# Optimization experiments

Measured on AMD Instinct MI355X. Metric: run time of the kernel, lower is better.

Reference implementation:

```python
import jax, jax.numpy as jnp
import numpy as np

B, N, C, H = 16, 577, 384, 6
ONE_DIM = 24
RPD = 2 * ONE_DIM - 1  # 47
NUM_CLS = 1
HEAD_DIM = C // H
SCALE = HEAD_DIM ** -0.5


def _build_rel_pos_index():
    # Faithful to the torch loop: tmp[dy - y + off, dx - x + off] with
    # torch's negative-index wraparound -> modulo RPD.
    off = ONE_DIM // 2
    qy = np.repeat(np.arange(ONE_DIM), ONE_DIM)  # (Np,) y of each query patch
    qx = np.tile(np.arange(ONE_DIM), ONE_DIM)    # (Np,) x of each query patch
    ky, kx = qy, qx                              # key patches use same grid
    ry = (ky[None, :] - qy[:, None] + off) % RPD
    rx = (kx[None, :] - qx[:, None] + off) % RPD
    return jnp.asarray(ry * RPD + rx, dtype=jnp.int32)  # (Np, Np)


def setup_inputs() -> dict:
    key = jax.random.key(0)
    k = jax.random.split(key, 6)
    x = jax.random.normal(k[0], (B, N, C), dtype=jnp.float32)
    qkv_w = jax.random.normal(k[1], (3 * C, C), dtype=jnp.float32) * 0.02
    qkv_b = jnp.zeros((3 * C,), dtype=jnp.float32)
    proj_w = jax.random.normal(k[2], (C, C), dtype=jnp.float32) * 0.02
    proj_b = jnp.zeros((C,), dtype=jnp.float32)
    rel_pos = jax.random.normal(k[3], (H, RPD * RPD), dtype=jnp.float32) * 0.02
    mask = jax.random.randint(k[4], (B, N, N), 0, 2, dtype=jnp.int32)
    return {
        "x": x, "qkv_w": qkv_w, "qkv_b": qkv_b,
        "proj_w": proj_w, "proj_b": proj_b, "rel_pos": rel_pos,
        "rel_pos_index": _build_rel_pos_index(),
        "mask": mask, "patch_attn": 1,
    }


def reference(x, qkv_w, qkv_b, proj_w, proj_b, rel_pos, rel_pos_index, mask, patch_attn):
    # qkv projection: torch Linear -> x @ W^T + b
    qkv = x @ qkv_w.T + qkv_b                               # (B, N, 3C)
    qkv = qkv.reshape(B, N, 3, H, HEAD_DIM).transpose(2, 0, 3, 1, 4)
    q, k, v = qkv[0], qkv[1], qkv[2]                        # (B, H, N, hd)

    attn = jnp.einsum("bhqd,bhkd->bhqk", q, k) * SCALE      # (B, H, N, N)

    if patch_attn:
        # gather per-head relative-position bias for patch tokens
        bias = rel_pos[:, rel_pos_index]                    # (H, Np, Np)
        attn = attn.at[:, :, NUM_CLS:, NUM_CLS:].add(bias)

    neg = jnp.finfo(attn.dtype).min
    attn = jnp.where(mask[:, None, :, :] == 0, neg, attn)   # broadcast over heads

    attn = jax.nn.softmax(attn, axis=-1)
    out = jnp.einsum("bhqk,bhkd->bhqd", attn, v)            # (B, H, N, hd)
    out = out.transpose(0, 2, 1, 3).reshape(B, N, C)
    out = out @ proj_w.T + proj_b
    return out
```

## Files before the change

kernel.cpp:

```cpp
#include <hip/hip_runtime.h>
#include <float.h>
#include <math.h>

#define NB 16
#define NN 577
#define NC 384
#define NH 6
#define ND 64
#define RPD2 2209
#define MTOT 9232
#define MPAD 9344
#define SCALE_ 0.125f
#define NEGBIG -3.0e38f
#define BSTRIDE 580
#define NKPAD 640

typedef __attribute__((ext_vector_type(8))) short bf16x8;
typedef __attribute__((ext_vector_type(4))) float f32x4;
typedef unsigned short u16;

#define MFMA16(a, b, c) __builtin_amdgcn_mfma_f32_16x16x32_bf16(a, b, c, 0, 0, 0)

#define SQA 3932160ull
#define OFF_QH 0ull
#define OFF_QL SQA
#define OFF_KH (2ull * SQA)
#define OFF_KL (3ull * SQA)
#define OFF_VTH (4ull * SQA)
#define OFF_VTL (5ull * SQA)
#define OFF_XH (6ull * SQA)
#define OFF_XL (6ull * SQA + 3588096ull)
#define OFF_WQH (6ull * SQA + 2ull * 3588096ull)
#define OFF_WQL (OFF_WQH + 442368ull)
#define OFF_WPH (OFF_WQL + 442368ull)
#define OFF_WPL (OFF_WPH + 147456ull)
#define OFF_BT  (OFF_WPL + 147456ull)
#define OFF_PM  (OFF_BT + 2007960ull)

static __device__ __forceinline__ u16 f2bf(float f) {
  unsigned u = __float_as_uint(f);
  u += 0x7fff + ((u >> 16) & 1);
  return (u16)(u >> 16);
}
static __device__ __forceinline__ float bf2f(u16 h) {
  return __uint_as_float((unsigned)h << 16);
}
static __device__ __forceinline__ void split2(float v, u16& hi, u16& lo) {
  hi = f2bf(v);
  lo = f2bf(v - bf2f(hi));
}
static __device__ __forceinline__ void gload16(const void* g, void* l) {
  __builtin_amdgcn_global_load_lds(
      (const __attribute__((address_space(1))) void*)g,
      (__attribute__((address_space(3))) void*)l, 16, 0, 0);
}

__global__ __launch_bounds__(256) void prep_k(
    const float* __restrict__ x, const float* __restrict__ wq,
    const float* __restrict__ wp, const int* __restrict__ mask,
    const float* __restrict__ rel_pos, const int* __restrict__ rel_idx,
    const int* __restrict__ patch, u16* __restrict__ ws)
{
  const int bidx = blockIdx.x;
  const int tid = threadIdx.x;

  if (bidx < 4080) {
    const int q = bidx * 256 + tid;
    float4 v = {0.f, 0.f, 0.f, 0.f};
    u16 *dh, *dl;
    if (q < 897024) {
      if (q < 886272) v = ((const float4*)x)[q];
      dh = ws + OFF_XH + 4ull * q;
      dl = ws + OFF_XL + 4ull * q;
    } else if (q < 1007616) {
      int t = q - 897024;
      v = ((const float4*)wq)[t];
      dh = ws + OFF_WQH + 4ull * t;
      dl = ws + OFF_WQL + 4ull * t;
    } else {
      int t = q - 1007616;
      v = ((const float4*)wp)[t];
      dh = ws + OFF_WPH + 4ull * t;
      dl = ws + OFF_WPL + 4ull * t;
    }
    ushort4 hh, ll;
    split2(v.x, hh.x, ll.x);
    split2(v.y, hh.y, ll.y);
    split2(v.z, hh.z, ll.z);
    split2(v.w, hh.w, ll.w);
    *(ushort4*)dh = hh;
    *(ushort4*)dl = ll;
  } else if (bidx < 6388) {
    unsigned* pm = (unsigned*)(ws + OFF_PM);
    const int pbid = bidx - 4080;
    const int wid = (pbid * 256 + tid) >> 6;
    const int lane = tid & 63;
    if (wid >= MTOT) return;
    const int* mr = mask + (size_t)wid * NN;
#pragma unroll
    for (int c = 0; c < 10; ++c) {
      int k = c * 64 + lane;
      int v = (k < NN) ? mr[k] : 0;
      unsigned long long bal = __ballot(v != 0);
      if (lane == 0) pm[wid * 20 + 2 * c] = (unsigned)bal;
      if (lane == 1) pm[wid * 20 + 2 * c + 1] = (unsigned)(bal >> 32);
    }
  } else {
    const int f = bidx - 6388;
    const int q = f % NN, h = f / NN;
    const int pa = *patch;
    u16* row = ws + OFF_BT + ((size_t)h * NN + q) * BSTRIDE;
    for (int kk = tid; kk < BSTRIDE; kk += 256) {
      float v = 0.f;
      if (pa && q >= 1 && kk >= 1 && kk < NN)
        v = rel_pos[h * RPD2 + rel_idx[(q - 1) * 576 + (kk - 1)]];
      row[kk] = f2bf(v);
    }
  }
}

__global__ __launch_bounds__(256, 5) void qkv_mfma_k(
    const u16* __restrict__ Xh, const u16* __restrict__ Xl,
    const u16* __restrict__ Wh, const u16* __restrict__ Wl,
    const float* __restrict__ bias, u16* __restrict__ ws)
{
  __shared__ u16 LB[16384];

#define pASH(bf) (LB + (bf) * 4096)
#define pASL(bf) (LB + 8192 + (bf) * 4096)

  const int tid = threadIdx.x;
  const int w = tid >> 6, l = tid & 63, lq = l & 15, lg = l >> 4;
  const int wm = (w >> 1) * 64, wn = (w & 1) * 32;

  const int o = blockIdx.x;
  const int xcd = o & 7, rank = o >> 3;
  const int wg = (xcd < 2) ? (xcd * 165 + rank)
                           : (330 + (xcd - 2) * 164 + rank);
  const int mb = (wg / 18) * 128;
  const int rbi = wg % 18;
  const int rb = rbi * 64;
  const int r0 = rb + wn;
  const int soff = (l >> 2) * 384 + (l & 3) * 8;

#define STAGE_A(k0_, bf_)                                                    \
  {                                                                          \
    _Pragma("unroll")                                                        \
    for (int j = 0; j < 2; ++j) {                                            \
      const int tr = 32 * w + 16 * j;                                        \
      const size_t ga = (size_t)(mb + tr) * 384 + (k0_) + soff;              \
      gload16(&Xh[ga], pASH(bf_) + tr * 32);                                 \
      gload16(&Xl[ga], pASL(bf_) + tr * 32);                                 \
    }                                                                        \
  }

  const size_t brow = (size_t)(r0 + lq) * 384 + 8 * lg;
#define BLOAD(k0_, BH_, BL_)                                                 \
  {                                                                          \
    _Pragma("unroll")                                                        \
    for (int nt = 0; nt < 2; ++nt) {                                         \
      BH_[nt] = *(const bf16x8*)&Wh[brow + (size_t)(16 * nt) * 384 + (k0_)]; \
      BL_[nt] = *(const bf16x8*)&Wl[brow + (size_t)(16 * nt) * 384 + (k0_)]; \
    }                                                                        \
  }

#define COMPUTE(bf_)                                                         \
  {                                                                          \
    _Pragma("unroll")                                                        \
    for (int mt = 0; mt < 4; ++mt) {                                         \
      bf16x8 ah = *(const bf16x8*)(pASH(bf_) + (wm + 16 * mt + lq) * 32 + 8 * lg); \
      bf16x8 al = *(const bf16x8*)(pASL(bf_) + (wm + 16 * mt + lq) * 32 + 8 * lg); \
      _Pragma("unroll")                                                      \
      for (int nt = 0; nt < 2; ++nt) {                                       \
        acc[mt][nt] = MFMA16(ah, bhf[nt], acc[mt][nt]);                      \
        acc[mt][nt] = MFMA16(ah, blf[nt], acc[mt][nt]);                      \
        acc[mt][nt] = MFMA16(al, bhf[nt], acc[mt][nt]);                      \
      }                                                                      \
    }                                                                        \
  }

  bf16x8 bhf[2], blf[2], nbh[2], nbl[2];
  BLOAD(0, bhf, blf);
  STAGE_A(0, 0);
  STAGE_A(32, 1);

  f32x4 acc[4][2];
#pragma unroll
  for (int nt = 0; nt < 2; ++nt) {
    float bv = bias[r0 + 16 * nt + lq];
#pragma unroll
    for (int mt = 0; mt < 4; ++mt) acc[mt][nt] = (f32x4){bv, bv, bv, bv};
  }

  for (int k = 0; k < 11; ++k) {
    asm volatile("s_waitcnt vmcnt(4)" ::: "memory");
    __builtin_amdgcn_sched_barrier(0);
    __builtin_amdgcn_s_barrier();
    __builtin_amdgcn_sched_barrier(0);
    const int bfb = k & 1;
    COMPUTE(bfb);
    __builtin_amdgcn_sched_barrier(0);
    __builtin_amdgcn_s_barrier();
    __builtin_amdgcn_sched_barrier(0);
    BLOAD(32 * (k + 1), nbh, nbl);
    if (k < 10) STAGE_A(32 * (k + 2), bfb);
#pragma unroll
    for (int nt = 0; nt < 2; ++nt) { bhf[nt] = nbh[nt]; blf[nt] = nbl[nt]; }
  }
  asm volatile("s_waitcnt vmcnt(0)" ::: "memory");
  __builtin_amdgcn_sched_barrier(0);
  __builtin_amdgcn_s_barrier();
  __builtin_amdgcn_sched_barrier(0);
  COMPUTE(1);

#undef COMPUTE
#undef BLOAD
#undef STAGE_A

  const int comp = rbi / 6;
  const int h = rbi % 6;

  if (comp != 2) {
#pragma unroll
    for (int mt = 0; mt < 4; ++mt)
#pragma unroll
      for (int r = 0; r < 4; ++r) {
        int m = mb + wm + 16 * mt + 4 * lg + r;
        if (m >= MTOT) continue;
        int bb = m / NN, nn = m - bb * NN;
        int bh = bb * NH + h;
#pragma unroll
        for (int nt = 0; nt < 2; ++nt) {
          int d = wn + 16 * nt + lq;
          float v = acc[mt][nt][r];
          u16 hi, lo;
          if (comp == 0) {
            v *= SCALE_;
            split2(v, hi, lo);
            size_t a = ((size_t)bh * NKPAD + nn) * 64 + d;
            ws[OFF_QH + a] = hi;
            ws[OFF_QL + a] = lo;
          } else {
            split2(v, hi, lo);
            size_t a = ((size_t)bh * NKPAD + nn) * 64 + d;
            ws[OFF_KH + a] = hi;
            ws[OFF_KL + a] = lo;
          }
        }
      }
  } else {
    __syncthreads();
    u16* scr = LB + w * 2304;
    const int mlane = mb + wm + l;
    const bool mv = mlane < MTOT;
    int bb = 0, nn = 0;
    if (mv) { bb = mlane / NN; nn = mlane - bb * NN; }
    const size_t vbase = (((size_t)(bb * NH + h) * 64 + wn)) * NKPAD + nn;

    for (int part = 0; part < 2; ++part) {
      u16* dst = ws + (part ? OFF_VTL : OFF_VTH);
#pragma unroll
      for (int nt = 0; nt < 2; ++nt)
#pragma unroll
        for (int mt = 0; mt < 4; ++mt) {
          ushort4 pk;
          u16 hi, lo;
          split2(acc[mt][nt][0], hi, lo); pk.x = part ? lo : hi;
          split2(acc[mt][nt][1], hi, lo); pk.y = part ? lo : hi;
          split2(acc[mt][nt][2], hi, lo); pk.z = part ? lo : hi;
          split2(acc[mt][nt][3], hi, lo); pk.w = part ? lo : hi;
          *(ushort4*)&scr[(16 * nt + lq) * 72 + 16 * mt + 4 * lg] = pk;
        }
      if (mv) {
        for (int i = 0; i < 32; ++i)
          dst[vbase + (size_t)i * NKPAD] = scr[i * 72 + l];
      }
    }
  }
#undef pASH
#undef pASL
}

__global__ __launch_bounds__(256, 2) void attn_k(
    const u16* __restrict__ Qh, const u16* __restrict__ Ql,
    const u16* __restrict__ Kh, const u16* __restrict__ Kl,
    const u16* __restrict__ Vth, const u16* __restrict__ Vtl,
    const u16* __restrict__ btbl, const unsigned* __restrict__ pm,
    u16* __restrict__ Oh, u16* __restrict__ Ol)
{
  __shared__ u16 Kth[2][4096], Ktl[2][4096];
  __shared__ u16 Vsh[2][4096], Vsl[2][4096];
  __shared__ u16 Ph[4][2048];

  const int tid = threadIdx.x;
  const int w = tid >> 6, l = tid & 63, lq = l & 15, lg = l >> 4;
  const int q0 = blockIdx.x * 128;
  const int h = blockIdx.y, b = blockIdx.z;
  const int bh = b * NH + h;
  const int qr0 = q0 + 32 * w + lq;
  const int qr1 = qr0 + 16;
  const int swz = (lq & 7) << 3;
  const int ln8 = l >> 3, lc8 = l & 7;
  const int koff = ln8 * 64 + ((lc8 ^ ln8) << 3);
  const int voff = ln8 * NKPAD + ((lc8 ^ ln8) << 3);

#define STAGE(ch, bf)                                                        \
  {                                                                          \
    const int kb_ = (ch) * 64;                                               \
    const size_t kgb = ((size_t)bh * NKPAD + kb_ + 16 * w) * 64 + koff;      \
    const size_t vgb = ((size_t)bh * 64 + 16 * w) * NKPAD + kb_ + voff;      \
    gload16(&Kh[kgb],              &Kth[bf][(16 * w) * 64]);                 \
    gload16(&Kh[kgb + 512],        &Kth[bf][(16 * w + 8) * 64]);             \
    gload16(&Kl[kgb],              &Ktl[bf][(16 * w) * 64]);                 \
    gload16(&Kl[kgb + 512],        &Ktl[bf][(16 * w + 8) * 64]);             \
    gload16(&Vth[vgb],             &Vsh[bf][(16 * w) * 64]);                 \
    gload16(&Vth[vgb + 8 * NKPAD], &Vsh[bf][(16 * w + 8) * 64]);             \
    gload16(&Vtl[vgb],             &Vsl[bf][(16 * w) * 64]);                 \
    gload16(&Vtl[vgb + 8 * NKPAD], &Vsl[bf][(16 * w + 8) * 64]);             \
  }

  STAGE(0, 0);

  const size_t qb0 = ((size_t)bh * NKPAD + qr0) * 64 + 8 * lg;
  const size_t qb1 = ((size_t)bh * NKPAD + qr1) * 64 + 8 * lg;
  bf16x8 q0h[2], q0l[2], q1h[2], q1l[2];
  q0h[0] = *(const bf16x8*)&Qh[qb0];
  q0h[1] = *(const bf16x8*)&Qh[qb0 + 32];
  q0l[0] = *(const bf16x8*)&Ql[qb0];
  q0l[1] = *(const bf16x8*)&Ql[qb0 + 32];
  q1h[0] = *(const bf16x8*)&Qh[qb1];
  q1h[1] = *(const bf16x8*)&Qh[qb1 + 32];
  q1l[0] = *(const bf16x8*)&Ql[qb1];
  q1l[1] = *(const bf16x8*)&Ql[qb1 + 32];

  const int gq0 = (qr0 < NN) ? qr0 : NN - 1;
  const int gq1 = (qr1 < NN) ? qr1 : NN - 1;
  const bool qv0 = qr0 < NN, qv1 = qr1 < NN;
  const unsigned* pmrow0 = pm + ((size_t)b * NN + gq0) * 20;
  const unsigned* pmrow1 = pm + ((size_t)b * NN + gq1) * 20;
  const size_t brow0 = ((size_t)h * NN + gq0) * BSTRIDE;
  const size_t brow1 = ((size_t)h * NN + gq1) * BSTRIDE;

  uint2 cM0, cM1, nM0, nM1;
  uint2 cB0[4], cB1[4], nB0[4], nB1[4];
  cM0 = *(const uint2*)&pmrow0[0];
  cM1 = *(const uint2*)&pmrow1[0];
#pragma unroll
  for (int t = 0; t < 4; ++t) {
    int kkb = 16 * t + 4 * lg;
    cB0[t] = (qv0 && kkb <= 576) ? *(const uint2*)&btbl[brow0 + kkb]
                                 : make_uint2(0u, 0u);
    cB1[t] = (qv1 && kkb <= 576) ? *(const uint2*)&btbl[brow1 + kkb]
                                 : make_uint2(0u, 0u);
  }

  float m_reg0 = NEGBIG, l_reg0 = 0.f;
  float m_reg1 = NEGBIG, l_reg1 = 0.f;
  f32x4 accO0[4] = {}, accO1[4] = {};

  for (int ch = 0; ch < 10; ++ch) {
    const int bf = ch & 1;
    __syncthreads();
    if (ch < 9) {
      nM0 = *(const uint2*)&pmrow0[2 * (ch + 1)];
      nM1 = *(const uint2*)&pmrow1[2 * (ch + 1)];
      const int kb2 = (ch + 1) * 64;
#pragma unroll
      for (int t = 0; t < 4; ++t) {
        int kkb = kb2 + 16 * t + 4 * lg;
        nB0[t] = (qv0 && kkb <= 576) ? *(const uint2*)&btbl[brow0 + kkb]
                                     : make_uint2(0u, 0u);
        nB1[t] = (qv1 && kkb <= 576) ? *(const uint2*)&btbl[brow1 + kkb]
                                     : make_uint2(0u, 0u);
      }
      STAGE(ch + 1, bf ^ 1);
    }

    unsigned long long m64_0 = (unsigned long long)cM0.x |
                               ((unsigned long long)cM0.y << 32);
    unsigned long long m64_1 = (unsigned long long)cM1.x |
                               ((unsigned long long)cM1.y << 32);

    float sv0[4][4], sv1[4][4];
    __builtin_amdgcn_s_setprio(1);
#pragma unroll
    for (int t = 0; t < 4; ++t) {
      f32x4 a0, a1;
      a0[0] = bf2f((u16)(cB0[t].x & 0xffff));
      a0[1] = bf2f((u16)(cB0[t].x >> 16));
      a0[2] = bf2f((u16)(cB0[t].y & 0xffff));
      a0[3] = bf2f((u16)(cB0[t].y >> 16));
      a1[0] = bf2f((u16)(cB1[t].x & 0xffff));
      a1[1] = bf2f((u16)(cB1[t].x >> 16));
      a1[2] = bf2f((u16)(cB1[t].y & 0xffff));
      a1[3] = bf2f((u16)(cB1[t].y >> 16));
      const int ar = (16 * t + lq) * 64;
#pragma unroll
      for (int ks = 0; ks < 2; ++ks) {
        const int c = (8 * lg + 32 * ks) ^ swz;
        bf16x8 ah = *(const bf16x8*)&Kth[bf][ar + c];
        bf16x8 al = *(const bf16x8*)&Ktl[bf][ar + c];
        a0 = MFMA16(ah, q0h[ks], a0);
        a0 = MFMA16(ah, q0l[ks], a0);
        a0 = MFMA16(al, q0h[ks], a0);
        a1 = MFMA16(ah, q1h[ks], a1);
        a1 = MFMA16(ah, q1l[ks], a1);
        a1 = MFMA16(al, q1h[ks], a1);
      }
#pragma unroll
      for (int r = 0; r < 4; ++r) { sv0[t][r] = a0[r]; sv1[t][r] = a1[r]; }
    }
    __builtin_amdgcn_s_setprio(0);

    {
      float cmax = NEGBIG;
#pragma unroll
      for (int t = 0; t < 4; ++t)
#pragma unroll
        for (int r = 0; r < 4; ++r) {
          int kl = 16 * t + 4 * lg + r;
          float s = ((m64_0 >> kl) & 1ull) ? sv0[t][r] : NEGBIG;
          sv0[t][r] = s;
          cmax = fmaxf(cmax, s);
        }
      cmax = fmaxf(cmax, __shfl_xor(cmax, 16));
      cmax = fmaxf(cmax, __shfl_xor(cmax, 32));
      float m_new = fmaxf(m_reg0, cmax);
      float fx = __expf(m_reg0 - m_new);
      float csum = 0.f;
#pragma unroll
      for (int t = 0; t < 4; ++t) {
        float e0 = __expf(sv0[t][0] - m_new);
        float e1 = __expf(sv0[t][1] - m_new);
        float e2 = __expf(sv0[t][2] - m_new);
        float e3 = __expf(sv0[t][3] - m_new);
        csum += e0 + e1 + e2 + e3;
        ushort4 ph;
        ph.x = f2bf(e0); ph.y = f2bf(e1); ph.z = f2bf(e2); ph.w = f2bf(e3);
        *(ushort4*)&Ph[w][lq * 64 + ((16 * t + 4 * lg) ^ swz)] = ph;
      }
      csum += __shfl_xor(csum, 16);
      csum += __shfl_xor(csum, 32);
      l_reg0 = l_reg0 * fx + csum;
      m_reg0 = m_new;
      float fxr[4];
#pragma unroll
      for (int r = 0; r < 4; ++r) fxr[r] = __shfl(fx, 4 * lg + r);
#pragma unroll
      for (int t = 0; t < 4; ++t) {
        accO0[t][0] *= fxr[0]; accO0[t][1] *= fxr[1];
        accO0[t][2] *= fxr[2]; accO0[t][3] *= fxr[3];
      }
    }
    {
      float cmax = NEGBIG;
#pragma unroll
      for (int t = 0; t < 4; ++t)
#pragma unroll
        for (int r = 0; r < 4; ++r) {
          int kl = 16 * t + 4 * lg + r;
          float s = ((m64_1 >> kl) & 1ull) ? sv1[t][r] : NEGBIG;
          sv1[t][r] = s;
          cmax = fmaxf(cmax, s);
        }
      cmax = fmaxf(cmax, __shfl_xor(cmax, 16));
      cmax = fmaxf(cmax, __shfl_xor(cmax, 32));
      float m_new = fmaxf(m_reg1, cmax);
      float fx = __expf(m_reg1 - m_new);
      float csum = 0.f;
#pragma unroll
      for (int t = 0; t < 4; ++t) {
        float e0 = __expf(sv1[t][0] - m_new);
        float e1 = __expf(sv1[t][1] - m_new);
        float e2 = __expf(sv1[t][2] - m_new);
        float e3 = __expf(sv1[t][3] - m_new);
        csum += e0 + e1 + e2 + e3;
        ushort4 ph;
        ph.x = f2bf(e0); ph.y = f2bf(e1); ph.z = f2bf(e2); ph.w = f2bf(e3);
        *(ushort4*)&Ph[w][(16 + lq) * 64 + ((16 * t + 4 * lg) ^ swz)] = ph;
      }
      csum += __shfl_xor(csum, 16);
      csum += __shfl_xor(csum, 32);
      l_reg1 = l_reg1 * fx + csum;
      m_reg1 = m_new;
      float fxr[4];
#pragma unroll
      for (int r = 0; r < 4; ++r) fxr[r] = __shfl(fx, 4 * lg + r);
#pragma unroll
      for (int t = 0; t < 4; ++t) {
        accO1[t][0] *= fxr[0]; accO1[t][1] *= fxr[1];
        accO1[t][2] *= fxr[2]; accO1[t][3] *= fxr[3];
      }
    }

    bf16x8 pa0[2], pa1[2];
#pragma unroll
    for (int ks = 0; ks < 2; ++ks) {
      int c = (8 * lg + 32 * ks) ^ swz;
      pa0[ks] = *(const bf16x8*)&Ph[w][lq * 64 + c];
      pa1[ks] = *(const bf16x8*)&Ph[w][(16 + lq) * 64 + c];
    }

    __builtin_amdgcn_s_setprio(1);
#pragma unroll
    for (int t = 0; t < 4; ++t) {
      const int vr = (16 * t + lq) * 64;
#pragma unroll
      for (int ks = 0; ks < 2; ++ks) {
        const int c = (8 * lg + 32 * ks) ^ swz;
        bf16x8 vh = *(const bf16x8*)&Vsh[bf][vr + c];
        bf16x8 vl = *(const bf16x8*)&Vsl[bf][vr + c];
        accO0[t] = MFMA16(pa0[ks], vh, accO0[t]);
        accO0[t] = MFMA16(pa0[ks], vl, accO0[t]);
        accO1[t] = MFMA16(pa1[ks], vh, accO1[t]);
        accO1[t] = MFMA16(pa1[ks], vl, accO1[t]);
      }
    }
    __builtin_amdgcn_s_setprio(0);

    if (ch < 9) {
      cM0 = nM0; cM1 = nM1;
#pragma unroll
      for (int t = 0; t < 4; ++t) { cB0[t] = nB0[t]; cB1[t] = nB1[t]; }
    }
  }
#undef STAGE

  float il0 = 1.f / l_reg0;
  float il1 = 1.f / l_reg1;
  float ilr0[4], ilr1[4];
#pragma unroll
  for (int r = 0; r < 4; ++r) {
    ilr0[r] = __shfl(il0, 4 * lg + r);
    ilr1[r] = __shfl(il1, 4 * lg + r);
  }
#pragma unroll
  for (int t = 0; t < 4; ++t)
#pragma unroll
    for (int r = 0; r < 4; ++r) {
      int g0 = q0 + 32 * w + 4 * lg + r;
      if (g0 < NN) {
        float v = accO0[t][r] * ilr0[r];
        u16 hi, lo;
        split2(v, hi, lo);
        size_t a = ((size_t)b * NN + g0) * NC + h * 64 + 16 * t + lq;
        Oh[a] = hi;
        Ol[a] = lo;
      }
      int g1 = g0 + 16;
      if (g1 < NN) {
        float v = accO1[t][r] * ilr1[r];
        u16 hi, lo;
        split2(v, hi, lo);
        size_t a = ((size_t)b * NN + g1) * NC + h * 64 + 16 * t + lq;
        Oh[a] = hi;
        Ol[a] = lo;
      }
    }
}

__global__ __launch_bounds__(256, 4) void proj_mfma_k(
    const u16* __restrict__ Ah, const u16* __restrict__ Al,
    const u16* __restrict__ Wh, const u16* __restrict__ Wl,
    const float* __restrict__ bias, float* __restrict__ out)
{
  __shared__ u16 Ash[2][2048], Asl[2][2048];

  const int tid = threadIdx.x;
  const int w = tid >> 6, l = tid & 63, lq = l & 15, lg = l >> 4;
  const int wm = (w >> 1) * 32, wn = (w & 1) * 32;
  const int mb = blockIdx.x * 64;
  const int rb = blockIdx.y * 64;
  const int r0 = rb + wn;
  const int soff = (l >> 2) * 384 + (l & 3) * 8;

#define STAGE_A(k0_, bf_)                                                    \
  {                                                                          \
    const int tr = 16 * w;                                                   \
    const size_t ga = (size_t)(mb + tr) * 384 + (k0_) + soff;                \
    gload16(&Ah[ga], &Ash[bf_][tr * 32]);                                    \
    gload16(&Al[ga], &Asl[bf_][tr * 32]);                                    \
  }

  const size_t brow = (size_t)(r0 + lq) * 384 + 8 * lg;
#define BLOAD(k0_, BH_, BL_)                                                 \
  {                                                                          \
    _Pragma("unroll")                                                        \
    for (int nt = 0; nt < 2; ++nt) {                                         \
      BH_[nt] = *(const bf16x8*)&Wh[brow + (size_t)(16 * nt) * 384 + (k0_)]; \
      BL_[nt] = *(const bf16x8*)&Wl[brow + (size_t)(16 * nt) * 384 + (k0_)]; \
    }                                                                        \
  }

#define COMPUTE(bf_)                                                         \
  {                                                                          \
    _Pragma("unroll")                                                        \
    for (int mt = 0; mt < 2; ++mt) {                                         \
      bf16x8 ah = *(const bf16x8*)&Ash[bf_][(wm + 16 * mt + lq) * 32 + 8 * lg]; \
      bf16x8 al = *(const bf16x8*)&Asl[bf_][(wm + 16 * mt + lq) * 32 + 8 * lg]; \
      _Pragma("unroll")                                                      \
      for (int nt = 0; nt < 2; ++nt) {                                       \
        acc[mt][nt] = MFMA16(ah, bhf[nt], acc[mt][nt]);                      \
        acc[mt][nt] = MFMA16(ah, blf[nt], acc[mt][nt]);                      \
        acc[mt][nt] = MFMA16(al, bhf[nt], acc[mt][nt]);                      \
      }                                                                      \
    }                                                                        \
  }

  bf16x8 bhf[2], blf[2], nbh[2], nbl[2];
  BLOAD(0, bhf, blf);
  STAGE_A(0, 0);
  STAGE_A(32, 1);

  f32x4 acc[2][2];
#pragma unroll
  for (int nt = 0; nt < 2; ++nt) {
    float bv = bias[r0 + 16 * nt + lq];
#pragma unroll
    for (int mt = 0; mt < 2; ++mt) acc[mt][nt] = (f32x4){bv, bv, bv, bv};
  }

  for (int k = 0; k < 11; ++k) {
    asm volatile("s_waitcnt vmcnt(2)" ::: "memory");
    __builtin_amdgcn_sched_barrier(0);
    __builtin_amdgcn_s_barrier();
    __builtin_amdgcn_sched_barrier(0);
    const int bfb = k & 1;
    COMPUTE(bfb);
    __builtin_amdgcn_sched_barrier(0);
    __builtin_amdgcn_s_barrier();
    __builtin_amdgcn_sched_barrier(0);
    BLOAD(32 * (k + 1), nbh, nbl);
    if (k < 10) STAGE_A(32 * (k + 2), bfb);
#pragma unroll
    for (int nt = 0; nt < 2; ++nt) { bhf[nt] = nbh[nt]; blf[nt] = nbl[nt]; }
  }
  asm volatile("s_waitcnt vmcnt(0)" ::: "memory");
  __builtin_amdgcn_sched_barrier(0);
  __builtin_amdgcn_s_barrier();
  __builtin_amdgcn_sched_barrier(0);
  COMPUTE(1);

#undef COMPUTE
#undef BLOAD
#undef STAGE_A

#pragma unroll
  for (int mt = 0; mt < 2; ++mt)
#pragma unroll
    for (int r = 0; r < 4; ++r) {
      int m = mb + wm + 16 * mt + 4 * lg + r;
      if (m >= MTOT) continue;
#pragma unroll
      for (int nt = 0; nt < 2; ++nt)
        out[(size_t)m * NC + r0 + 16 * nt + lq] = acc[mt][nt][r];
    }
}

extern "C" void kernel_launch(void* const* d_in, const int* in_sizes, int n_in,
                              void* d_out, int out_size, void* d_ws, size_t ws_size,
                              hipStream_t stream) {
  const float* x       = (const float*)d_in[0];
  const float* qkv_w   = (const float*)d_in[1];
  const float* qkv_b   = (const float*)d_in[2];
  const float* proj_w  = (const float*)d_in[3];
  const float* proj_b  = (const float*)d_in[4];
  const float* rel_pos = (const float*)d_in[5];
  const int*   rel_idx = (const int*)d_in[6];
  const int*   mask    = (const int*)d_in[7];
  const int*   patch   = (const int*)d_in[8];
  float* out = (float*)d_out;
  u16* W16 = (u16*)d_ws;

  unsigned* pmp = (unsigned*)(W16 + OFF_PM);
  u16* btblp = W16 + OFF_BT;

  prep_k<<<9850, 256, 0, stream>>>(x, qkv_w, proj_w, mask, rel_pos, rel_idx,
                                   patch, W16);
  qkv_mfma_k<<<1314, 256, 0, stream>>>(
      W16 + OFF_XH, W16 + OFF_XL, W16 + OFF_WQH, W16 + OFF_WQL, qkv_b, W16);
  attn_k<<<dim3(5, NH, NB), 256, 0, stream>>>(
      W16 + OFF_QH, W16 + OFF_QL, W16 + OFF_KH, W16 + OFF_KL,
      W16 + OFF_VTH, W16 + OFF_VTL, btblp, pmp,
      W16 + OFF_XH, W16 + OFF_XL);
  proj_mfma_k<<<dim3(146, 6), 256, 0, stream>>>(
      W16 + OFF_XH, W16 + OFF_XL, W16 + OFF_WPH, W16 + OFF_WPL, proj_b, out);
}
```

Measured before the change: 151.5 us.

## Move mask/bias prep into QKV GEMM launch and restructure GEMM k-loop pipelining

The mask bit-packing and relative-position bias table construction move from the prep kernel into extra blocks of the QKV GEMM launch, so they run alongside the GEMM instead of before it. The prep kernel now only splits x and the weights into bf16 hi/lo. Both GEMM kernels change their k-loop to a fully unrolled 12-step double buffer with one barrier per step, issuing the next tile's loads before computing the current one. The loop now waits for all loads to finish (vmcnt(0)) at each step, which reduces overlap between memory loads and MFMA work.

```diff
diff --git a/kernel.cpp b/kernel.cpp
--- a/kernel.cpp
+++ b/kernel.cpp
@@ -57,83 +57,85 @@
 
 __global__ __launch_bounds__(256) void prep_k(
     const float* __restrict__ x, const float* __restrict__ wq,
-    const float* __restrict__ wp, const int* __restrict__ mask,
+    const float* __restrict__ wp, u16* __restrict__ ws)
+{
+  const int q = blockIdx.x * 256 + threadIdx.x;
+  float4 v = {0.f, 0.f, 0.f, 0.f};
+  u16 *dh, *dl;
+  if (q < 897024) {
+    if (q < 886272) v = ((const float4*)x)[q];
+    dh = ws + OFF_XH + 4ull * q;
+    dl = ws + OFF_XL + 4ull * q;
+  } else if (q < 1007616) {
+    int t = q - 897024;
+    v = ((const float4*)wq)[t];
+    dh = ws + OFF_WQH + 4ull * t;
+    dl = ws + OFF_WQL + 4ull * t;
+  } else {
+    int t = q - 1007616;
+    v = ((const float4*)wp)[t];
+    dh = ws + OFF_WPH + 4ull * t;
+    dl = ws + OFF_WPL + 4ull * t;
+  }
+  ushort4 hh, ll;
+  split2(v.x, hh.x, ll.x);
+  split2(v.y, hh.y, ll.y);
+  split2(v.z, hh.z, ll.z);
+  split2(v.w, hh.w, ll.w);
+  *(ushort4*)dh = hh;
+  *(ushort4*)dl = ll;
+}
+
+__global__ __launch_bounds__(256, 5) void qkv_mfma_k(
+    const u16* __restrict__ Xh, const u16* __restrict__ Xl,
+    const u16* __restrict__ Wh, const u16* __restrict__ Wl,
+    const float* __restrict__ bias, const int* __restrict__ mask,
     const float* __restrict__ rel_pos, const int* __restrict__ rel_idx,
     const int* __restrict__ patch, u16* __restrict__ ws)
 {
-  const int bidx = blockIdx.x;
+  __shared__ u16 LB[16384];
+
+  const int bid = blockIdx.x;
   const int tid = threadIdx.x;
 
-  if (bidx < 4080) {
-    const int q = bidx * 256 + tid;
-    float4 v = {0.f, 0.f, 0.f, 0.f};
-    u16 *dh, *dl;
-    if (q < 897024) {
-      if (q < 886272) v = ((const float4*)x)[q];
-      dh = ws + OFF_XH + 4ull * q;
-      dl = ws + OFF_XL + 4ull * q;
-    } else if (q < 1007616) {
-      int t = q - 897024;
-      v = ((const float4*)wq)[t];
-      dh = ws + OFF_WQH + 4ull * t;
-      dl = ws + OFF_WQL + 4ull * t;
+  if (bid >= 1314) {
+    if (bid < 3622) {
+      unsigned* pm = (unsigned*)(ws + OFF_PM);
+      const int pbid = bid - 1314;
+      const int wid = (pbid * 256 + tid) >> 6;
+      const int lane = tid & 63;
+      if (wid >= MTOT) return;
+      const int* mr = mask + (size_t)wid * NN;
+#pragma unroll
+      for (int c = 0; c < 10; ++c) {
+        int k = c * 64 + lane;
+        int v = (k < NN) ? mr[k] : 0;
+        unsigned long long bal = __ballot(v != 0);
+        if (lane == 0) pm[wid * 20 + 2 * c] = (unsigned)bal;
+        if (lane == 1) pm[wid * 20 + 2 * c + 1] = (unsigned)(bal >> 32);
+      }
     } else {
-      int t = q - 1007616;
-      v = ((const float4*)wp)[t];
-      dh = ws + OFF_WPH + 4ull * t;
-      dl = ws + OFF_WPL + 4ull * t;
-    }
-    ushort4 hh, ll;
-    split2(v.x, hh.x, ll.x);
-    split2(v.y, hh.y, ll.y);
-    split2(v.z, hh.z, ll.z);
-    split2(v.w, hh.w, ll.w);
-    *(ushort4*)dh = hh;
-    *(ushort4*)dl = ll;
-  } else if (bidx < 6388) {
-    unsigned* pm = (unsigned*)(ws + OFF_PM);
-    const int pbid = bidx - 4080;
-    const int wid = (pbid * 256 + tid) >> 6;
-    const int lane = tid & 63;
-    if (wid >= MTOT) return;
-    const int* mr = mask + (size_t)wid * NN;
-#pragma unroll
-    for (int c = 0; c < 10; ++c) {
-      int k = c * 64 + lane;
-      int v = (k < NN) ? mr[k] : 0;
-      unsigned long long bal = __ballot(v != 0);
-      if (lane == 0) pm[wid * 20 + 2 * c] = (unsigned)bal;
-      if (lane == 1) pm[wid * 20 + 2 * c + 1] = (unsigned)(bal >> 32);
-    }
-  } else {
-    const int f = bidx - 6388;
-    const int q = f % NN, h = f / NN;
-    const int pa = *patch;
-    u16* row = ws + OFF_BT + ((size_t)h * NN + q) * BSTRIDE;
-    for (int kk = tid; kk < BSTRIDE; kk += 256) {
-      float v = 0.f;
-      if (pa && q >= 1 && kk >= 1 && kk < NN)
-        v = rel_pos[h * RPD2 + rel_idx[(q - 1) * 576 + (kk - 1)]];
-      row[kk] = f2bf(v);
-    }
-  }
-}
-
-__global__ __launch_bounds__(256, 5) void qkv_mfma_k(
-    const u16* __restrict__ Xh, const u16* __restrict__ Xl,
-    const u16* __restrict__ Wh, const u16* __restrict__ Wl,
-    const float* __restrict__ bias, u16* __restrict__ ws)
-{
-  __shared__ u16 LB[16384];
+      const int f = bid - 3622;
+      const int q = f % NN, h = f / NN;
+      const int pa = *patch;
+      u16* row = ws + OFF_BT + ((size_t)h * NN + q) * BSTRIDE;
+      for (int kk = tid; kk < BSTRIDE; kk += 256) {
+        float v = 0.f;
+        if (pa && q >= 1 && kk >= 1 && kk < NN)
+          v = rel_pos[h * RPD2 + rel_idx[(q - 1) * 576 + (kk - 1)]];
+        row[kk] = f2bf(v);
+      }
+    }
+    return;
+  }
 
 #define pASH(bf) (LB + (bf) * 4096)
 #define pASL(bf) (LB + 8192 + (bf) * 4096)
 
-  const int tid = threadIdx.x;
   const int w = tid >> 6, l = tid & 63, lq = l & 15, lg = l >> 4;
   const int wm = (w >> 1) * 64, wn = (w & 1) * 32;
 
-  const int o = blockIdx.x;
+  const int o = bid;
   const int xcd = o & 7, rank = o >> 3;
   const int wg = (xcd < 2) ? (xcd * 165 + rank)
                            : (330 + (xcd - 2) * 164 + rank);
@@ -164,7 +166,7 @@
     }                                                                        \
   }
 
-#define COMPUTE(bf_)                                                         \
+#define COMPUTE(bf_, BH_, BL_)                                               \
   {                                                                          \
     _Pragma("unroll")                                                        \
     for (int mt = 0; mt < 4; ++mt) {                                         \
@@ -172,17 +174,16 @@
       bf16x8 al = *(const bf16x8*)(pASL(bf_) + (wm + 16 * mt + lq) * 32 + 8 * lg); \
       _Pragma("unroll")                                                      \
       for (int nt = 0; nt < 2; ++nt) {                                       \
-        acc[mt][nt] = MFMA16(ah, bhf[nt], acc[mt][nt]);                      \
-        acc[mt][nt] = MFMA16(ah, blf[nt], acc[mt][nt]);                      \
-        acc[mt][nt] = MFMA16(al, bhf[nt], acc[mt][nt]);                      \
+        acc[mt][nt] = MFMA16(ah, BH_[nt], acc[mt][nt]);                      \
+        acc[mt][nt] = MFMA16(ah, BL_[nt], acc[mt][nt]);                      \
+        acc[mt][nt] = MFMA16(al, BH_[nt], acc[mt][nt]);                      \
       }                                                                      \
     }                                                                        \
   }
 
-  bf16x8 bhf[2], blf[2], nbh[2], nbl[2];
-  BLOAD(0, bhf, blf);
+  bf16x8 bh2[2][2], bl2[2][2];
   STAGE_A(0, 0);
-  STAGE_A(32, 1);
+  BLOAD(0, bh2[0], bl2[0]);
 
   f32x4 acc[4][2];
 #pragma unroll
@@ -192,26 +193,21 @@
     for (int mt = 0; mt < 4; ++mt) acc[mt][nt] = (f32x4){bv, bv, bv, bv};
   }
 
-  for (int k = 0; k < 11; ++k) {
+#pragma unroll
+  for (int k = 0; k < 12; ++k) {
+    const int cur = k & 1;
     asm volatile("s_waitcnt vmcnt(4)" ::: "memory");
     __builtin_amdgcn_sched_barrier(0);
     __builtin_amdgcn_s_barrier();
     __builtin_amdgcn_sched_barrier(0);
-    const int bfb = k & 1;
-    COMPUTE(bfb);
+    asm volatile("s_waitcnt vmcnt(0)" ::: "memory");
     __builtin_amdgcn_sched_barrier(0);
-    __builtin_amdgcn_s_barrier();
-    __builtin_amdgcn_sched_barrier(0);
-    BLOAD(32 * (k + 1), nbh, nbl);
-    if (k < 10) STAGE_A(32 * (k + 2), bfb);
-#pragma unroll
-    for (int nt = 0; nt < 2; ++nt) { bhf[nt] = nbh[nt]; blf[nt] = nbl[nt]; }
-  }
-  asm volatile("s_waitcnt vmcnt(0)" ::: "memory");
-  __builtin_amdgcn_sched_barrier(0);
-  __builtin_amdgcn_s_barrier();
-  __builtin_amdgcn_sched_barrier(0);
-  COMPUTE(1);
+    if (k < 11) {
+      STAGE_A(32 * (k + 1), cur ^ 1);
+      BLOAD(32 * (k + 1), bh2[cur ^ 1], bl2[cur ^ 1]);
+    }
+    COMPUTE(cur, bh2[cur], bl2[cur]);
+  }
 
 #undef COMPUTE
 #undef BLOAD
@@ -592,7 +588,7 @@
     }                                                                        \
   }
 
-#define COMPUTE(bf_)                                                         \
+#define COMPUTE(bf_, BH_, BL_)                                               \
   {                                                                          \
     _Pragma("unroll")                                                        \
     for (int mt = 0; mt < 2; ++mt) {                                         \
@@ -600,17 +596,16 @@
       bf16x8 al = *(const bf16x8*)&Asl[bf_][(wm + 16 * mt + lq) * 32 + 8 * lg]; \
       _Pragma("unroll")                                                      \
       for (int nt = 0; nt < 2; ++nt) {                                       \
-        acc[mt][nt] = MFMA16(ah, bhf[nt], acc[mt][nt]);                      \
-        acc[mt][nt] = MFMA16(ah, blf[nt], acc[mt][nt]);                      \
-        acc[mt][nt] = MFMA16(al, bhf[nt], acc[mt][nt]);                      \
+        acc[mt][nt] = MFMA16(ah, BH_[nt], acc[mt][nt]);                      \
+        acc[mt][nt] = MFMA16(ah, BL_[nt], acc[mt][nt]);                      \
+        acc[mt][nt] = MFMA16(al, BH_[nt], acc[mt][nt]);                      \
       }                                                                      \
     }                                                                        \
   }
 
-  bf16x8 bhf[2], blf[2], nbh[2], nbl[2];
-  BLOAD(0, bhf, blf);
+  bf16x8 bh2[2][2], bl2[2][2];
   STAGE_A(0, 0);
-  STAGE_A(32, 1);
+  BLOAD(0, bh2[0], bl2[0]);
 
   f32x4 acc[2][2];
 #pragma unroll
@@ -620,26 +615,21 @@
     for (int mt = 0; mt < 2; ++mt) acc[mt][nt] = (f32x4){bv, bv, bv, bv};
   }
 
-  for (int k = 0; k < 11; ++k) {
-    asm volatile("s_waitcnt vmcnt(2)" ::: "memory");
+#pragma unroll
+  for (int k = 0; k < 12; ++k) {
+    const int cur = k & 1;
+    asm volatile("s_waitcnt vmcnt(4)" ::: "memory");
     __builtin_amdgcn_sched_barrier(0);
     __builtin_amdgcn_s_barrier();
     __builtin_amdgcn_sched_barrier(0);
-    const int bfb = k & 1;
-    COMPUTE(bfb);
+    asm volatile("s_waitcnt vmcnt(0)" ::: "memory");
     __builtin_amdgcn_sched_barrier(0);
-    __builtin_amdgcn_s_barrier();
-    __builtin_amdgcn_sched_barrier(0);
-    BLOAD(32 * (k + 1), nbh, nbl);
-    if (k < 10) STAGE_A(32 * (k + 2), bfb);
-#pragma unroll
-    for (int nt = 0; nt < 2; ++nt) { bhf[nt] = nbh[nt]; blf[nt] = nbl[nt]; }
-  }
-  asm volatile("s_waitcnt vmcnt(0)" ::: "memory");
-  __builtin_amdgcn_sched_barrier(0);
-  __builtin_amdgcn_s_barrier();
-  __builtin_amdgcn_sched_barrier(0);
-  COMPUTE(1);
+    if (k < 11) {
+      STAGE_A(32 * (k + 1), cur ^ 1);
+      BLOAD(32 * (k + 1), bh2[cur ^ 1], bl2[cur ^ 1]);
+    }
+    COMPUTE(cur, bh2[cur], bl2[cur]);
+  }
 
 #undef COMPUTE
 #undef BLOAD
@@ -675,10 +665,10 @@
   unsigned* pmp = (unsigned*)(W16 + OFF_PM);
   u16* btblp = W16 + OFF_BT;
 
-  prep_k<<<9850, 256, 0, stream>>>(x, qkv_w, proj_w, mask, rel_pos, rel_idx,
-                                   patch, W16);
-  qkv_mfma_k<<<1314, 256, 0, stream>>>(
-      W16 + OFF_XH, W16 + OFF_XL, W16 + OFF_WQH, W16 + OFF_WQL, qkv_b, W16);
+  prep_k<<<4080, 256, 0, stream>>>(x, qkv_w, proj_w, W16);
+  qkv_mfma_k<<<7084, 256, 0, stream>>>(
+      W16 + OFF_XH, W16 + OFF_XL, W16 + OFF_WQH, W16 + OFF_WQL, qkv_b,
+      mask, rel_pos, rel_idx, patch, W16);
   attn_k<<<dim3(5, NH, NB), 256, 0, stream>>>(
       W16 + OFF_QH, W16 + OFF_QL, W16 + OFF_KH, W16 + OFF_KL,
       W16 + OFF_VTH, W16 + OFF_VTL, btblp, pmp,
```

Result: faster. 148.0 us (-2.3%).
